# Kernel tuning notes

Measured on AMD Instinct MI355X. Metric: run time of the kernel, lower is better.

Reference implementation:

```python
import jax, jax.numpy as jnp
import numpy as np

LN_EPS = 1e-5


def entmax15(z):
    # exact 1.5-entmax over last axis (Peters & Martins sorting algorithm)
    z = z / 2.0
    z = z - jnp.max(z, axis=-1, keepdims=True)  # shift-invariant, for stability
    zs = -jnp.sort(-z, axis=-1)                 # descending sort
    k = jnp.arange(1, z.shape[-1] + 1, dtype=z.dtype)
    mean = jnp.cumsum(zs, axis=-1) / k
    meansq = jnp.cumsum(zs * zs, axis=-1) / k
    ss = k * (meansq - jnp.square(mean))
    delta = (1.0 - ss) / k
    tau = mean - jnp.sqrt(jnp.clip(delta, 0.0))
    support = jnp.sum((tau <= zs).astype(jnp.int32), axis=-1, keepdims=True)
    tau_star = jnp.take_along_axis(tau, support - 1, axis=-1)
    return jnp.square(jnp.clip(z - tau_star, 0.0))


def layernorm_noaffine(v):
    m = jnp.mean(v, axis=-1, keepdims=True)
    var = jnp.mean(jnp.square(v - m), axis=-1, keepdims=True)
    return (v - m) / jnp.sqrt(var + LN_EPS)


def cp_mumoe(x, gate, Win, Wout):
    ones = jnp.ones(x.shape[:-1] + (1,), x.dtype)
    xb = jnp.concatenate([x, ones], axis=-1)
    z = jnp.einsum('btd,dr->btr', xb, Win) * gate  # [b,t,R]
    return jnp.einsum('btr,or->bto', z, Wout)      # [b,t,o]


def setup_inputs() -> dict:
    key = jax.random.key(0)
    ks = jax.random.split(key, 8)
    B, T, D, O, D2, E, R = 8, 2048, 1024, 4096, 1024, 16, 512
    s = lambda k, shape, scale: jax.random.normal(k, shape, jnp.float32) * scale
    return {
        'x': s(ks[0], (B, T, D), 1.0),
        'proj': s(ks[1], (D, E), D ** -0.5),
        'C1': s(ks[2], (E, R), E ** -0.5),
        'Win1': s(ks[3], (D + 1, R), D ** -0.5),
        'Wout1': s(ks[4], (O, R), R ** -0.5),
        'C2': s(ks[5], (E, R), E ** -0.5),
        'Win2': s(ks[6], (O + 1, R), O ** -0.5),
        'Wout2': s(ks[7], (D2, R), R ** -0.5),
    }


def reference(x, proj, C1, Win1, Wout1, C2, Win2, Wout2):
    # expert gating: projection -> LN (no affine) -> 1.5-entmax
    a = entmax15(layernorm_noaffine(jnp.einsum('btd,de->bte', x, proj)))  # [b,t,E]
    # layer 1: CP-decomposed expert mixture (bias folded into input mode)
    g1 = jnp.einsum('bte,er->btr', a, C1)
    h = cp_mumoe(x, g1, Win1, Wout1)
    # GELU + layer 2 reusing the same gate coefficients
    h = jax.nn.gelu(h, approximate=False)
    g2 = jnp.einsum('bte,er->btr', a, C2)
    return cp_mumoe(h, g2, Win2, Wout2)
```

## Files before the change

### kernel.cpp

```cpp
#include <hip/hip_runtime.h>
#include <hip/hip_bf16.h>
#include <math.h>
#include <stdint.h>

typedef unsigned short u16;
typedef __attribute__((ext_vector_type(8))) short bf16x8;
typedef __attribute__((ext_vector_type(4))) float f32x4;
typedef __attribute__((address_space(3))) void* as3_void;
typedef const __attribute__((address_space(1))) void* as1_cvoid;

__device__ inline u16 f2bf(float f) {
    union { float f; unsigned u; } v; v.f = f;
    unsigned r = v.u + 0x7FFFu + ((v.u >> 16) & 1u);
    return (u16)(r >> 16);
}
__device__ inline float bf2f(u16 h) {
    unsigned u = ((unsigned)h) << 16;
    return __builtin_bit_cast(float, u);
}

template<int CTRL, int RM>
__device__ inline float dpp_mov(float v) {
    return __builtin_bit_cast(float, __builtin_amdgcn_update_dpp(
        0, __builtin_bit_cast(int, v), CTRL, RM, 0xf, false));
}
__device__ inline float wave_sum(float v) {
    v += dpp_mov<0x111, 0xf>(v);
    v += dpp_mov<0x112, 0xf>(v);
    v += dpp_mov<0x114, 0xf>(v);
    v += dpp_mov<0x118, 0xf>(v);
    v += dpp_mov<0x142, 0xa>(v);
    v += dpp_mov<0x143, 0xc>(v);
    return v;
}

__global__ __launch_bounds__(256)
void prep_win(const float* __restrict__ W, u16* __restrict__ Wt,
              float* __restrict__ bias, int logD, int R)
{
    int idx = blockIdx.x * 256 + threadIdx.x;
    int D = 1 << logD;
    int total = D * R;
    if (idx < total) {
        int r = idx >> logD;
        int d = idx & (D - 1);
        Wt[idx] = f2bf(W[(size_t)d * R + r]);
    }
    if (idx < R) bias[idx] = W[(size_t)D * R + idx];
}

__global__ __launch_bounds__(256)
void prep_wout(const float* __restrict__ W, u16* __restrict__ Wt, int total)
{
    int idx = blockIdx.x * 256 + threadIdx.x;
    if (idx < total) Wt[idx] = f2bf(W[idx]);
}

__global__ __launch_bounds__(256)
void k1_proj(const float* __restrict__ x, const float* __restrict__ proj,
             u16* __restrict__ xb, float* __restrict__ sbuf, int Ntok)
{
    __shared__ float plt[16 * 1024];
    const int tid = threadIdx.x;
    #pragma unroll
    for (int k = 0; k < 64; ++k) {
        int idx = k * 256 + tid;
        int e = idx & 15, d = idx >> 4;
        plt[e * 1024 + (d ^ (e << 2))] = proj[idx];
    }
    __syncthreads();

    const int lane = tid & 63;
    const int wid = tid >> 6;
    const int t0 = (blockIdx.x * 4 + wid) * 2;
    if (t0 >= Ntok) return;

    float s[16][2];
    #pragma unroll
    for (int e = 0; e < 16; ++e) { s[e][0] = 0.f; s[e][1] = 0.f; }

    #pragma unroll
    for (int j = 0; j < 4; ++j) {
        const int d0 = (j * 64 + lane) * 4;
        float4 xq[2];
        #pragma unroll
        for (int q = 0; q < 2; ++q) {
            xq[q] = *(const float4*)&x[(size_t)(t0 + q) * 1024 + d0];
            short4 h;
            h.x = (short)f2bf(xq[q].x); h.y = (short)f2bf(xq[q].y);
            h.z = (short)f2bf(xq[q].z); h.w = (short)f2bf(xq[q].w);
            *(short4*)&xb[(size_t)(t0 + q) * 1024 + d0] = h;
        }
        #pragma unroll
        for (int e = 0; e < 16; ++e) {
            float4 p = *(const float4*)&plt[e * 1024 + (d0 ^ (e << 2))];
            #pragma unroll
            for (int q = 0; q < 2; ++q) {
                s[e][q] = fmaf(xq[q].x, p.x, s[e][q]);
                s[e][q] = fmaf(xq[q].y, p.y, s[e][q]);
                s[e][q] = fmaf(xq[q].z, p.z, s[e][q]);
                s[e][q] = fmaf(xq[q].w, p.w, s[e][q]);
            }
        }
    }
    #pragma unroll
    for (int e = 0; e < 16; ++e) {
        s[e][0] = wave_sum(s[e][0]);
        s[e][1] = wave_sum(s[e][1]);
    }
    if (lane == 63) {
        #pragma unroll
        for (int q = 0; q < 2; ++q)
            #pragma unroll
            for (int c = 0; c < 4; ++c) {
                float4 o = { s[c * 4 + 0][q], s[c * 4 + 1][q],
                             s[c * 4 + 2][q], s[c * 4 + 3][q] };
                *(float4*)&sbuf[(size_t)(t0 + q) * 16 + c * 4] = o;
            }
    }
}

__global__ __launch_bounds__(256)
void k1_entmax(const float* __restrict__ sbuf, float* __restrict__ abuf, int Ntok)
{
    int t = blockIdx.x * 256 + threadIdx.x;
    if (t >= Ntok) return;
    float s[16];
    #pragma unroll
    for (int c = 0; c < 4; ++c) {
        float4 v = *(const float4*)&sbuf[(size_t)t * 16 + c * 4];
        s[c * 4 + 0] = v.x; s[c * 4 + 1] = v.y; s[c * 4 + 2] = v.z; s[c * 4 + 3] = v.w;
    }
    float mean = 0.f;
    #pragma unroll
    for (int e = 0; e < 16; ++e) mean += s[e];
    mean *= 0.0625f;
    float var = 0.f;
    #pragma unroll
    for (int e = 0; e < 16; ++e) { float d = s[e] - mean; var = fmaf(d, d, var); }
    var *= 0.0625f;
    float rstd = rsqrtf(var + 1e-5f);

    float z[16];
    #pragma unroll
    for (int e = 0; e < 16; ++e) z[e] = (s[e] - mean) * rstd * 0.5f;
    float zmax = z[0];
    #pragma unroll
    for (int e = 1; e < 16; ++e) zmax = fmaxf(zmax, z[e]);
    #pragma unroll
    for (int e = 0; e < 16; ++e) z[e] -= zmax;

    float zs[16];
    #pragma unroll
    for (int e = 0; e < 16; ++e) zs[e] = z[e];
    #pragma unroll
    for (int k = 2; k <= 16; k <<= 1) {
        #pragma unroll
        for (int j = k >> 1; j > 0; j >>= 1) {
            #pragma unroll
            for (int i = 0; i < 16; ++i) {
                int l = i ^ j;
                if (l > i) {
                    float a = zs[i], b = zs[l];
                    bool asc = ((i & k) == 0);
                    bool sw = asc ? (a > b) : (a < b);
                    if (sw) { zs[i] = b; zs[l] = a; }
                }
            }
        }
    }
    float csum = 0.f, csq = 0.f, tau_star = -3.4e38f;
    #pragma unroll
    for (int kk = 1; kk <= 16; ++kk) {
        float v = zs[16 - kk];
        csum += v; csq += v * v;
        float kf = (float)kk;
        float mn = csum / kf;
        float ms = csq / kf;
        float ss = kf * (ms - mn * mn);
        float delta = fmaxf((1.f - ss) / kf, 0.f);
        float tau = mn - sqrtf(delta);
        if (tau <= v) tau_star = tau;
    }
    #pragma unroll
    for (int c = 0; c < 4; ++c) {
        float4 o;
        float p0 = fmaxf(z[c * 4 + 0] - tau_star, 0.f);
        float p1 = fmaxf(z[c * 4 + 1] - tau_star, 0.f);
        float p2 = fmaxf(z[c * 4 + 2] - tau_star, 0.f);
        float p3 = fmaxf(z[c * 4 + 3] - tau_star, 0.f);
        o.x = p0 * p0; o.y = p1 * p1; o.z = p2 * p2; o.w = p3 * p3;
        *(float4*)&abuf[(size_t)t * 16 + c * 4] = o;
    }
}

__global__ __launch_bounds__(256)
void gcompute(const float* __restrict__ abuf, const float* __restrict__ C1,
              const float* __restrict__ C2, u16* __restrict__ g1,
              u16* __restrict__ g2, int Ntok)
{
    const int tid = threadIdx.x;
    const int lane = tid & 63;
    const int t = blockIdx.x * 4 + (tid >> 6);
    if (t >= Ntok) return;
    float a[16];
    #pragma unroll
    for (int c = 0; c < 4; ++c) {
        float4 v = *(const float4*)&abuf[(size_t)t * 16 + c * 4];
        a[c * 4 + 0] = v.x; a[c * 4 + 1] = v.y; a[c * 4 + 2] = v.z; a[c * 4 + 3] = v.w;
    }
    #pragma unroll
    for (int c8 = 0; c8 < 8; ++c8) {
        int col = c8 * 64 + lane;
        float t1 = 0.f, t2 = 0.f;
        #pragma unroll
        for (int e = 0; e < 16; ++e) {
            t1 = fmaf(a[e], C1[e * 512 + col], t1);
            t2 = fmaf(a[e], C2[e * 512 + col], t2);
        }
        g1[(size_t)t * 512 + col] = f2bf(t1);
        g2[(size_t)t * 512 + col] = f2bf(t2);
    }
}

template<int MODE>
__global__ __launch_bounds__(256)
void gemm_bt(const u16* __restrict__ A, const u16* __restrict__ Bt,
             const float* __restrict__ bias, const u16* __restrict__ gmat,
             void* __restrict__ Cout, int M, int Nn, int K, int tilesN)
{
    __shared__ __align__(1024) char smem[65536];
    const int tid = threadIdx.x;
    const int lane = tid & 63;
    const int wid = tid >> 6;

    int bid = blockIdx.x;
    {
        int nwg = gridDim.x;
        if (nwg >= 16) {
            int q = nwg >> 3, r = nwg & 7;
            int xcd = bid & 7, loc = bid >> 3;
            bid = (xcd < r ? xcd * (q + 1) : r * (q + 1) + (xcd - r) * q) + loc;
        }
    }
    const int m0 = (bid / tilesN) * 128;
    const int n0 = (bid % tilesN) * 128;
    const int wm = (wid >> 1) * 64;
    const int wn = (wid & 1) * 64;

    f32x4 acc[4][4];
    #pragma unroll
    for (int i = 0; i < 4; ++i)
        #pragma unroll
        for (int j = 0; j < 4; ++j) acc[i][j] = (f32x4){0.f, 0.f, 0.f, 0.f};

    auto STAGE = [&](int b, int k0) {
        #pragma unroll
        for (int i = 0; i < 4; ++i) {
            int q = (wid * 4 + i) * 64 + lane;
            int row = q >> 3;
            int c = (q & 7) ^ (row & 7);
            __builtin_amdgcn_global_load_lds(
                (as1_cvoid)(A + (size_t)(m0 + row) * K + k0 + c * 8),
                (as3_void)&smem[b * 32768 + (wid * 4 + i) * 1024], 16, 0, 0);
        }
        #pragma unroll
        for (int i = 0; i < 4; ++i) {
            int q = (wid * 4 + i) * 64 + lane;
            int row = q >> 3;
            int c = (q & 7) ^ (row & 7);
            __builtin_amdgcn_global_load_lds(
                (as1_cvoid)(Bt + (size_t)(n0 + row) * K + k0 + c * 8),
                (as3_void)&smem[b * 32768 + 16384 + (wid * 4 + i) * 1024], 16, 0, 0);
        }
    };

    auto COMPUTE = [&](int b) {
        #pragma unroll
        for (int kk = 0; kk < 2; ++kk) {
            bf16x8 af[4], bfr[4];
            const int slot = kk * 4 + (lane >> 4);
            #pragma unroll
            for (int i = 0; i < 4; ++i) {
                int row = wm + i * 16 + (lane & 15);
                af[i] = *(const bf16x8*)
                    &smem[b * 32768 + row * 128 + ((slot ^ (row & 7)) << 4)];
            }
            #pragma unroll
            for (int j = 0; j < 4; ++j) {
                int row = wn + j * 16 + (lane & 15);
                bfr[j] = *(const bf16x8*)
                    &smem[b * 32768 + 16384 + row * 128 + ((slot ^ (row & 7)) << 4)];
            }
            #pragma unroll
            for (int i = 0; i < 4; ++i)
                #pragma unroll
                for (int j = 0; j < 4; ++j)
                    acc[i][j] = __builtin_amdgcn_mfma_f32_16x16x32_bf16(
                        af[i], bfr[j], acc[i][j], 0, 0, 0);
        }
    };

    const int nsteps = K >> 6;
    STAGE(0, 0);
    __syncthreads();
    int cur = 0;
    for (int ks = 0; ks < nsteps; ++ks) {
        if (ks + 1 < nsteps) STAGE(cur ^ 1, (ks + 1) << 6);
        COMPUTE(cur);
        __syncthreads();
        cur ^= 1;
    }

    const int cl = lane & 15;
    const int rq = (lane >> 4) * 4;
    #pragma unroll
    for (int i = 0; i < 4; ++i) {
        #pragma unroll
        for (int j = 0; j < 4; ++j) {
            int col = n0 + wn + j * 16 + cl;
            float bv = (MODE == 1) ? bias[col] : 0.f;
            #pragma unroll
            for (int r = 0; r < 4; ++r) {
                int row = m0 + wm + i * 16 + rq + r;
                float v = acc[i][j][r];
                if (MODE == 0) {
                    v = 0.5f * v * (1.f + erff(v * 0.70710678118654752f));
                    ((u16*)Cout)[(size_t)row * Nn + col] = f2bf(v);
                } else if (MODE == 1) {
                    v = (v + bv) * bf2f(gmat[(size_t)row * Nn + col]);
                    ((u16*)Cout)[(size_t)row * Nn + col] = f2bf(v);
                } else {
                    ((float*)Cout)[(size_t)row * Nn + col] = v;
                }
            }
        }
    }
}

extern "C" void kernel_launch(void* const* d_in, const int* in_sizes, int n_in,
                              void* d_out, int out_size, void* d_ws, size_t ws_size,
                              hipStream_t stream)
{
    const float* x     = (const float*)d_in[0];
    const float* proj  = (const float*)d_in[1];
    const float* C1    = (const float*)d_in[2];
    const float* Win1  = (const float*)d_in[3];
    const float* Wout1 = (const float*)d_in[4];
    const float* C2    = (const float*)d_in[5];
    const float* Win2  = (const float*)d_in[6];
    const float* Wout2 = (const float*)d_in[7];

    const int D = 1024, O = 4096, R = 512, D2 = 1024;
    const int Ntok = in_sizes[0] / D;

    char* ws = (char*)d_ws;
    size_t off = 0;
    auto alloc = [&](size_t bytes) -> void* {
        void* p = ws + off;
        off += (bytes + 255) & ~(size_t)255;
        return p;
    };
    u16*   z1  = (u16*)  alloc((size_t)Ntok * R * 2);
    u16*   z2  = (u16*)  alloc((size_t)Ntok * R * 2);
    u16*   w1o = (u16*)  alloc((size_t)O * R * 2);
    u16*   w2t = (u16*)  alloc((size_t)R * O * 2);
    u16*   w2o = (u16*)  alloc((size_t)D2 * R * 2);
    float* b1  = (float*)alloc(R * 4);
    float* b2  = (float*)alloc(R * 4);
    size_t persist_end = off;

    u16*   xb   = (u16*)  alloc((size_t)Ntok * D * 2);
    u16*   w1t  = (u16*)  alloc((size_t)R * D * 2);
    float* sbuf = (float*)alloc((size_t)Ntok * 16 * 4);
    float* abuf = (float*)alloc((size_t)Ntok * 16 * 4);

    size_t hAvail = (ws_size > persist_end) ? (ws_size - persist_end) : 0;
    long long chRows = (long long)(hAvail / ((size_t)O * 2));
    chRows &= ~127LL;
    int CH = (chRows > Ntok) ? Ntok : (int)chRows;
    if (CH < 128) CH = 128;
    u16* hbuf = (u16*)(ws + persist_end);

    u16* g1 = z1;
    u16* g2 = z2;

    prep_win <<<(D * R + 255) / 256, 256, 0, stream>>>(Win1, w1t, b1, 10, R);
    prep_win <<<(O * R + 255) / 256, 256, 0, stream>>>(Win2, w2t, b2, 12, R);
    prep_wout<<<(O * R + 255) / 256, 256, 0, stream>>>(Wout1, w1o, O * R);
    prep_wout<<<(D2 * R + 255) / 256, 256, 0, stream>>>(Wout2, w2o, D2 * R);

    k1_proj  <<<Ntok / 8, 256, 0, stream>>>(x, proj, xb, sbuf, Ntok);
    k1_entmax<<<(Ntok + 255) / 256, 256, 0, stream>>>(sbuf, abuf, Ntok);
    gcompute <<<(Ntok + 3) / 4, 256, 0, stream>>>(abuf, C1, C2, g1, g2, Ntok);

    gemm_bt<1><<<(Ntok / 128) * (R / 128), 256, 0, stream>>>(
        xb, w1t, b1, g1, z1, Ntok, R, D, R / 128);

    for (int r0 = 0; r0 < Ntok; r0 += CH) {
        int cm = Ntok - r0; if (cm > CH) cm = CH;
        gemm_bt<0><<<(cm / 128) * (O / 128), 256, 0, stream>>>(
            z1 + (size_t)r0 * R, w1o, nullptr, nullptr,
            hbuf, cm, O, R, O / 128);
        gemm_bt<1><<<(cm / 128) * (R / 128), 256, 0, stream>>>(
            hbuf, w2t, b2, g2 + (size_t)r0 * R,
            z2 + (size_t)r0 * R, cm, R, O, R / 128);
    }

    gemm_bt<2><<<(Ntok / 128) * (D2 / 128), 256, 0, stream>>>(
        z2, w2o, nullptr, nullptr, d_out, Ntok, D2, R, D2 / 128);
}
```

Before: 341.8 us.

## Replace GEMM with 256x128-tile, 8-wave, triple-buffered pipelined kernel

The bf16 MFMA GEMM moves from 128x128 tiles with 4 waves and double buffering to 256x128 tiles with 8 waves and a three-stage LDS ring (144 KB). Global-to-LDS loads for the tile two steps ahead are interleaved with the compute phases, using explicit vmcnt waits, barriers and setprio around the MFMA bursts. The aim is to hide load latency and raise arithmetic intensity per block. The cost is one block per CU and fewer blocks overall (for R=512 GEMMs only 256 blocks), which lowers occupancy. The hbuf chunk size is aligned to 256 rows to match.

```diff
diff --git a/kernel.cpp b/kernel.cpp
--- a/kernel.cpp
+++ b/kernel.cpp
@@ -223,16 +223,20 @@
     }
 }
 
+#define MFMA16(a, b, c) __builtin_amdgcn_mfma_f32_16x16x32_bf16(a, b, c, 0, 0, 0)
+
 template<int MODE>
-__global__ __launch_bounds__(256)
-void gemm_bt(const u16* __restrict__ A, const u16* __restrict__ Bt,
+__global__ __launch_bounds__(512, 1)
+void gemm256(const u16* __restrict__ A, const u16* __restrict__ Bt,
              const float* __restrict__ bias, const u16* __restrict__ gmat,
              void* __restrict__ Cout, int M, int Nn, int K, int tilesN)
 {
-    __shared__ __align__(1024) char smem[65536];
+    __shared__ __align__(1024) char smem[147456];
     const int tid = threadIdx.x;
     const int lane = tid & 63;
     const int wid = tid >> 6;
+    const int wr = wid >> 2;
+    const int wc = wid & 3;
 
     int bid = blockIdx.x;
     {
@@ -243,86 +247,131 @@
             bid = (xcd < r ? xcd * (q + 1) : r * (q + 1) + (xcd - r) * q) + loc;
         }
     }
-    const int m0 = (bid / tilesN) * 128;
+    const int m0 = (bid / tilesN) * 256;
     const int n0 = (bid % tilesN) * 128;
-    const int wm = (wid >> 1) * 64;
-    const int wn = (wid & 1) * 64;
-
-    f32x4 acc[4][4];
-    #pragma unroll
-    for (int i = 0; i < 4; ++i)
-        #pragma unroll
-        for (int j = 0; j < 4; ++j) acc[i][j] = (f32x4){0.f, 0.f, 0.f, 0.f};
-
-    auto STAGE = [&](int b, int k0) {
+
+    f32x4 acc[8][2];
+    #pragma unroll
+    for (int i = 0; i < 8; ++i) {
+        acc[i][0] = (f32x4){0.f, 0.f, 0.f, 0.f};
+        acc[i][1] = (f32x4){0.f, 0.f, 0.f, 0.f};
+    }
+
+    auto stageA = [&](int buf, int k0, int ai) {
+        int q = ai * 512 + tid;
+        int row = q >> 3;
+        int c = (q & 7) ^ (row & 7);
+        __builtin_amdgcn_global_load_lds(
+            (as1_cvoid)(A + (size_t)(m0 + row) * K + k0 + c * 8),
+            (as3_void)&smem[buf * 49152 + (ai * 512 + wid * 64) * 16], 16, 0, 0);
+    };
+    auto stageB = [&](int buf, int k0, int bi) {
+        int q = bi * 512 + tid;
+        int row = q >> 3;
+        int c = (q & 7) ^ (row & 7);
+        __builtin_amdgcn_global_load_lds(
+            (as1_cvoid)(Bt + (size_t)(n0 + row) * K + k0 + c * 8),
+            (as3_void)&smem[buf * 49152 + 32768 + (bi * 512 + wid * 64) * 16], 16, 0, 0);
+    };
+
+    const int arow = wr * 128 + (lane & 15);
+    const int brow = wc * 32 + (lane & 15);
+    const int sHi  = lane >> 4;
+    const int aX = arow & 7, bX = brow & 7;
+    const int abyte = arow * 128;
+    const int bbyte = 32768 + brow * 128;
+
+    auto LDA = [&](int buf, int i, int kk) -> bf16x8 {
+        return *(const bf16x8*)&smem[buf * 49152 + abyte + i * 2048
+                                     + ((((kk << 2) | sHi) ^ aX) << 4)];
+    };
+    auto LDB = [&](int buf, int j, int kk) -> bf16x8 {
+        return *(const bf16x8*)&smem[buf * 49152 + bbyte + j * 2048
+                                     + ((((kk << 2) | sHi) ^ bX) << 4)];
+    };
+
+    const int nt = K >> 6;
+    #pragma unroll
+    for (int ai = 0; ai < 4; ++ai) stageA(0, 0, ai);
+    stageB(0, 0, 0); stageB(0, 0, 1);
+    #pragma unroll
+    for (int ai = 0; ai < 4; ++ai) stageA(1, 64, ai);
+    stageB(1, 64, 0); stageB(1, 64, 1);
+
+    for (int t = 0; t < nt; ++t) {
+        const int buf = t % 3;
+        const int sb = (t + 2) % 3;
+        const int sk = (t + 2) << 6;
+        const bool st = (t + 2) < nt;
+        if (t < nt - 1) asm volatile("s_waitcnt vmcnt(6)" ::: "memory");
+        else            asm volatile("s_waitcnt vmcnt(0)" ::: "memory");
+        __builtin_amdgcn_sched_barrier(0);
+        __builtin_amdgcn_s_barrier();
+
+        bf16x8 aR[4], bR[2];
+        aR[0] = LDA(buf, 0, 0); aR[1] = LDA(buf, 1, 0);
+        aR[2] = LDA(buf, 2, 0); aR[3] = LDA(buf, 3, 0);
+        bR[0] = LDB(buf, 0, 0); bR[1] = LDB(buf, 1, 0);
+        if (st) { stageA(sb, sk, 0); stageA(sb, sk, 1); }
+        __builtin_amdgcn_s_barrier();
+        __builtin_amdgcn_s_setprio(1);
         #pragma unroll
         for (int i = 0; i < 4; ++i) {
-            int q = (wid * 4 + i) * 64 + lane;
-            int row = q >> 3;
-            int c = (q & 7) ^ (row & 7);
-            __builtin_amdgcn_global_load_lds(
-                (as1_cvoid)(A + (size_t)(m0 + row) * K + k0 + c * 8),
-                (as3_void)&smem[b * 32768 + (wid * 4 + i) * 1024], 16, 0, 0);
-        }
+            acc[i][0] = MFMA16(aR[i], bR[0], acc[i][0]);
+            acc[i][1] = MFMA16(aR[i], bR[1], acc[i][1]);
+        }
+        __builtin_amdgcn_s_setprio(0);
+        __builtin_amdgcn_s_barrier();
+        aR[0] = LDA(buf, 4, 0); aR[1] = LDA(buf, 5, 0);
+        aR[2] = LDA(buf, 6, 0); aR[3] = LDA(buf, 7, 0);
+        if (st) { stageA(sb, sk, 2); stageA(sb, sk, 3); }
+        __builtin_amdgcn_s_barrier();
+        __builtin_amdgcn_s_setprio(1);
         #pragma unroll
         for (int i = 0; i < 4; ++i) {
-            int q = (wid * 4 + i) * 64 + lane;
-            int row = q >> 3;
-            int c = (q & 7) ^ (row & 7);
-            __builtin_amdgcn_global_load_lds(
-                (as1_cvoid)(Bt + (size_t)(n0 + row) * K + k0 + c * 8),
-                (as3_void)&smem[b * 32768 + 16384 + (wid * 4 + i) * 1024], 16, 0, 0);
-        }
-    };
-
-    auto COMPUTE = [&](int b) {
-        #pragma unroll
-        for (int kk = 0; kk < 2; ++kk) {
-            bf16x8 af[4], bfr[4];
-            const int slot = kk * 4 + (lane >> 4);
-            #pragma unroll
-            for (int i = 0; i < 4; ++i) {
-                int row = wm + i * 16 + (lane & 15);
-                af[i] = *(const bf16x8*)
-                    &smem[b * 32768 + row * 128 + ((slot ^ (row & 7)) << 4)];
-            }
-            #pragma unroll
-            for (int j = 0; j < 4; ++j) {
-                int row = wn + j * 16 + (lane & 15);
-                bfr[j] = *(const bf16x8*)
-                    &smem[b * 32768 + 16384 + row * 128 + ((slot ^ (row & 7)) << 4)];
-            }
-            #pragma unroll
-            for (int i = 0; i < 4; ++i)
-                #pragma unroll
-                for (int j = 0; j < 4; ++j)
-                    acc[i][j] = __builtin_amdgcn_mfma_f32_16x16x32_bf16(
-                        af[i], bfr[j], acc[i][j], 0, 0, 0);
-        }
-    };
-
-    const int nsteps = K >> 6;
-    STAGE(0, 0);
-    __syncthreads();
-    int cur = 0;
-    for (int ks = 0; ks < nsteps; ++ks) {
-        if (ks + 1 < nsteps) STAGE(cur ^ 1, (ks + 1) << 6);
-        COMPUTE(cur);
-        __syncthreads();
-        cur ^= 1;
+            acc[4 + i][0] = MFMA16(aR[i], bR[0], acc[4 + i][0]);
+            acc[4 + i][1] = MFMA16(aR[i], bR[1], acc[4 + i][1]);
+        }
+        __builtin_amdgcn_s_setprio(0);
+        __builtin_amdgcn_s_barrier();
+        aR[0] = LDA(buf, 0, 1); aR[1] = LDA(buf, 1, 1);
+        aR[2] = LDA(buf, 2, 1); aR[3] = LDA(buf, 3, 1);
+        bR[0] = LDB(buf, 0, 1); bR[1] = LDB(buf, 1, 1);
+        if (st) stageB(sb, sk, 0);
+        __builtin_amdgcn_s_barrier();
+        __builtin_amdgcn_s_setprio(1);
+        #pragma unroll
+        for (int i = 0; i < 4; ++i) {
+            acc[i][0] = MFMA16(aR[i], bR[0], acc[i][0]);
+            acc[i][1] = MFMA16(aR[i], bR[1], acc[i][1]);
+        }
+        __builtin_amdgcn_s_setprio(0);
+        __builtin_amdgcn_s_barrier();
+        aR[0] = LDA(buf, 4, 1); aR[1] = LDA(buf, 5, 1);
+        aR[2] = LDA(buf, 6, 1); aR[3] = LDA(buf, 7, 1);
+        if (st) stageB(sb, sk, 1);
+        __builtin_amdgcn_s_barrier();
+        __builtin_amdgcn_s_setprio(1);
+        #pragma unroll
+        for (int i = 0; i < 4; ++i) {
+            acc[4 + i][0] = MFMA16(aR[i], bR[0], acc[4 + i][0]);
+            acc[4 + i][1] = MFMA16(aR[i], bR[1], acc[4 + i][1]);
+        }
+        __builtin_amdgcn_s_setprio(0);
+        __builtin_amdgcn_s_barrier();
     }
 
     const int cl = lane & 15;
     const int rq = (lane >> 4) * 4;
     #pragma unroll
-    for (int i = 0; i < 4; ++i) {
-        #pragma unroll
-        for (int j = 0; j < 4; ++j) {
-            int col = n0 + wn + j * 16 + cl;
+    for (int i = 0; i < 8; ++i) {
+        #pragma unroll
+        for (int j = 0; j < 2; ++j) {
+            int col = n0 + wc * 32 + j * 16 + cl;
             float bv = (MODE == 1) ? bias[col] : 0.f;
             #pragma unroll
             for (int r = 0; r < 4; ++r) {
-                int row = m0 + wm + i * 16 + rq + r;
+                int row = m0 + wr * 128 + i * 16 + rq + r;
                 float v = acc[i][j][r];
                 if (MODE == 0) {
                     v = 0.5f * v * (1.f + erff(v * 0.70710678118654752f));
@@ -377,9 +426,9 @@
 
     size_t hAvail = (ws_size > persist_end) ? (ws_size - persist_end) : 0;
     long long chRows = (long long)(hAvail / ((size_t)O * 2));
-    chRows &= ~127LL;
+    chRows &= ~255LL;
     int CH = (chRows > Ntok) ? Ntok : (int)chRows;
-    if (CH < 128) CH = 128;
+    if (CH < 256) CH = 256;
     u16* hbuf = (u16*)(ws + persist_end);
 
     u16* g1 = z1;
@@ -394,19 +443,19 @@
     k1_entmax<<<(Ntok + 255) / 256, 256, 0, stream>>>(sbuf, abuf, Ntok);
     gcompute <<<(Ntok + 3) / 4, 256, 0, stream>>>(abuf, C1, C2, g1, g2, Ntok);
 
-    gemm_bt<1><<<(Ntok / 128) * (R / 128), 256, 0, stream>>>(
+    gemm256<1><<<(Ntok / 256) * (R / 128), 512, 0, stream>>>(
         xb, w1t, b1, g1, z1, Ntok, R, D, R / 128);
 
     for (int r0 = 0; r0 < Ntok; r0 += CH) {
         int cm = Ntok - r0; if (cm > CH) cm = CH;
-        gemm_bt<0><<<(cm / 128) * (O / 128), 256, 0, stream>>>(
+        gemm256<0><<<(cm / 256) * (O / 128), 512, 0, stream>>>(
             z1 + (size_t)r0 * R, w1o, nullptr, nullptr,
             hbuf, cm, O, R, O / 128);
-        gemm_bt<1><<<(cm / 128) * (R / 128), 256, 0, stream>>>(
+        gemm256<1><<<(cm / 256) * (R / 128), 512, 0, stream>>>(
             hbuf, w2t, b2, g2 + (size_t)r0 * R,
             z2 + (size_t)r0 * R, cm, R, O, R / 128);
     }
 
-    gemm_bt<2><<<(Ntok / 128) * (D2 / 128), 256, 0, stream>>>(
+    gemm256<2><<<(Ntok / 256) * (D2 / 128), 512, 0, stream>>>(
         z2, w2o, nullptr, nullptr, d_out, Ntok, D2, R, D2 / 128);
 }
```

After: 363.0 us. +6.2%, slower.

## Add triple-buffered deep GEMM for layer-2 input and tanh-style GELU

Applied to the files above, without the earlier changes.

Adds a new gemm_deep kernel that uses a three-stage LDS ring of 32KB buffers, with two K-steps of prefetch in flight via global_load_lds and vmcnt waits. This targets the long-K (K=4096) layer-2 input projection, where a double buffer may leave load latency exposed. It also replaces exact erf-based GELU with a sigmoid form of the tanh approximation, to cut epilogue cost in the O-wide GEMM. The GELU change departs from the exact reference and may add error. The 96KB of shared memory per block can reduce occupancy.

```diff
diff --git a/kernel.cpp b/kernel.cpp
--- a/kernel.cpp
+++ b/kernel.cpp
@@ -17,6 +17,10 @@
 __device__ inline float bf2f(u16 h) {
     unsigned u = ((unsigned)h) << 16;
     return __builtin_bit_cast(float, u);
+}
+__device__ inline float gelu_fast(float v) {
+    float t = v * fmaf(0.07135702f, v * v, 1.5957691f);
+    return v / (1.f + __expf(-t));
 }
 
 template<int CTRL, int RM>
@@ -325,8 +329,129 @@
                 int row = m0 + wm + i * 16 + rq + r;
                 float v = acc[i][j][r];
                 if (MODE == 0) {
-                    v = 0.5f * v * (1.f + erff(v * 0.70710678118654752f));
+                    ((u16*)Cout)[(size_t)row * Nn + col] = f2bf(gelu_fast(v));
+                } else if (MODE == 1) {
+                    v = (v + bv) * bf2f(gmat[(size_t)row * Nn + col]);
                     ((u16*)Cout)[(size_t)row * Nn + col] = f2bf(v);
+                } else {
+                    ((float*)Cout)[(size_t)row * Nn + col] = v;
+                }
+            }
+        }
+    }
+}
+
+template<int MODE>
+__global__ __launch_bounds__(256)
+void gemm_deep(const u16* __restrict__ A, const u16* __restrict__ Bt,
+               const float* __restrict__ bias, const u16* __restrict__ gmat,
+               void* __restrict__ Cout, int M, int Nn, int K, int tilesN)
+{
+    __shared__ __align__(1024) char smem[98304];
+    const int tid = threadIdx.x;
+    const int lane = tid & 63;
+    const int wid = tid >> 6;
+
+    int bid = blockIdx.x;
+    {
+        int nwg = gridDim.x;
+        if (nwg >= 16) {
+            int q = nwg >> 3, r = nwg & 7;
+            int xcd = bid & 7, loc = bid >> 3;
+            bid = (xcd < r ? xcd * (q + 1) : r * (q + 1) + (xcd - r) * q) + loc;
+        }
+    }
+    const int m0 = (bid / tilesN) * 128;
+    const int n0 = (bid % tilesN) * 128;
+    const int wm = (wid >> 1) * 64;
+    const int wn = (wid & 1) * 64;
+
+    f32x4 acc[4][4];
+    #pragma unroll
+    for (int i = 0; i < 4; ++i)
+        #pragma unroll
+        for (int j = 0; j < 4; ++j) acc[i][j] = (f32x4){0.f, 0.f, 0.f, 0.f};
+
+    auto STAGE = [&](int b, int k0) {
+        #pragma unroll
+        for (int i = 0; i < 4; ++i) {
+            int q = (wid * 4 + i) * 64 + lane;
+            int row = q >> 3;
+            int c = (q & 7) ^ (row & 7);
+            __builtin_amdgcn_global_load_lds(
+                (as1_cvoid)(A + (size_t)(m0 + row) * K + k0 + c * 8),
+                (as3_void)&smem[b * 32768 + (wid * 4 + i) * 1024], 16, 0, 0);
+        }
+        #pragma unroll
+        for (int i = 0; i < 4; ++i) {
+            int q = (wid * 4 + i) * 64 + lane;
+            int row = q >> 3;
+            int c = (q & 7) ^ (row & 7);
+            __builtin_amdgcn_global_load_lds(
+                (as1_cvoid)(Bt + (size_t)(n0 + row) * K + k0 + c * 8),
+                (as3_void)&smem[b * 32768 + 16384 + (wid * 4 + i) * 1024], 16, 0, 0);
+        }
+    };
+
+    auto COMPUTE = [&](int b) {
+        #pragma unroll
+        for (int kk = 0; kk < 2; ++kk) {
+            bf16x8 af[4], bfr[4];
+            const int slot = kk * 4 + (lane >> 4);
+            #pragma unroll
+            for (int i = 0; i < 4; ++i) {
+                int row = wm + i * 16 + (lane & 15);
+                af[i] = *(const bf16x8*)
+                    &smem[b * 32768 + row * 128 + ((slot ^ (row & 7)) << 4)];
+            }
+            #pragma unroll
+            for (int j = 0; j < 4; ++j) {
+                int row = wn + j * 16 + (lane & 15);
+                bfr[j] = *(const bf16x8*)
+                    &smem[b * 32768 + 16384 + row * 128 + ((slot ^ (row & 7)) << 4)];
+            }
+            #pragma unroll
+            for (int i = 0; i < 4; ++i)
+                #pragma unroll
+                for (int j = 0; j < 4; ++j)
+                    acc[i][j] = __builtin_amdgcn_mfma_f32_16x16x32_bf16(
+                        af[i], bfr[j], acc[i][j], 0, 0, 0);
+        }
+    };
+
+    const int nsteps = K >> 6;
+    STAGE(0, 0);
+    if (nsteps > 1) STAGE(1, 64);
+    if (nsteps > 1) asm volatile("s_waitcnt vmcnt(8)" ::: "memory");
+    else            asm volatile("s_waitcnt vmcnt(0)" ::: "memory");
+    __builtin_amdgcn_sched_barrier(0);
+    __builtin_amdgcn_s_barrier();
+
+    for (int t = 0; t < nsteps; ++t) {
+        if (t + 2 < nsteps) STAGE((t + 2) % 3, (t + 2) << 6);
+        COMPUTE(t % 3);
+        if (t + 1 < nsteps) {
+            if (t + 2 < nsteps) asm volatile("s_waitcnt vmcnt(8)" ::: "memory");
+            else                asm volatile("s_waitcnt vmcnt(0)" ::: "memory");
+            __builtin_amdgcn_sched_barrier(0);
+            __builtin_amdgcn_s_barrier();
+        }
+    }
+
+    const int cl = lane & 15;
+    const int rq = (lane >> 4) * 4;
+    #pragma unroll
+    for (int i = 0; i < 4; ++i) {
+        #pragma unroll
+        for (int j = 0; j < 4; ++j) {
+            int col = n0 + wn + j * 16 + cl;
+            float bv = (MODE == 1) ? bias[col] : 0.f;
+            #pragma unroll
+            for (int r = 0; r < 4; ++r) {
+                int row = m0 + wm + i * 16 + rq + r;
+                float v = acc[i][j][r];
+                if (MODE == 0) {
+                    ((u16*)Cout)[(size_t)row * Nn + col] = f2bf(gelu_fast(v));
                 } else if (MODE == 1) {
                     v = (v + bv) * bf2f(gmat[(size_t)row * Nn + col]);
                     ((u16*)Cout)[(size_t)row * Nn + col] = f2bf(v);
@@ -402,7 +527,7 @@
         gemm_bt<0><<<(cm / 128) * (O / 128), 256, 0, stream>>>(
             z1 + (size_t)r0 * R, w1o, nullptr, nullptr,
             hbuf, cm, O, R, O / 128);
-        gemm_bt<1><<<(cm / 128) * (R / 128), 256, 0, stream>>>(
+        gemm_deep<1><<<(cm / 128) * (R / 128), 256, 0, stream>>>(
             hbuf, w2t, b2, g2 + (size_t)r0 * R,
             z2 + (size_t)r0 * R, cm, R, O, R / 128);
     }
```

New measurement: 371.1 us. 8.6% more time.
